# Performance work log

Measured on AMD Instinct MI355X. Metric: run time of the kernel, lower is better.

## Reference

```python
import jax, jax.numpy as jnp
import numpy as np

C64 = jnp.complex64


def _rot_mats(theta):
    """Return (RX, RY, RZ) 2x2 complex matrices for half-angle convention."""
    c = jnp.cos(theta / 2).astype(C64)
    s = jnp.sin(theta / 2).astype(C64)
    i = jnp.asarray(1j, C64)
    rx = jnp.stack([jnp.stack([c, -i * s]), jnp.stack([-i * s, c])])
    ry = jnp.stack([jnp.stack([c, -s]), jnp.stack([s, c])])
    e = jnp.exp(-i * theta.astype(C64) / 2)
    z0 = jnp.asarray(0.0, C64)
    rz = jnp.stack([jnp.stack([e, z0]), jnp.stack([z0, jnp.conj(e)])])
    return rx, ry, rz


def _apply_1q(state, U, wire):
    # state: [N,2,2,2,2]; apply U on qubit axis (1+wire)
    state = jnp.moveaxis(state, 1 + wire, 4)
    state = jnp.einsum('ab,nijkb->nijka', U, state)
    return jnp.moveaxis(state, 4, 1 + wire)


def _apply_cnot(state, ctrl, tgt):
    state = jnp.moveaxis(state, (1 + ctrl, 1 + tgt), (3, 4))
    s0 = state[..., 0, :]
    s1 = state[..., 1, ::-1]  # flip target where control=1
    state = jnp.stack([s0, s1], axis=3)
    return jnp.moveaxis(state, (3, 4), (1 + ctrl, 1 + tgt))


def _quanvolution(x, q_params):
    B = x.shape[0]
    img = x.reshape(B, 28, 28)
    # 2x2 non-overlapping patches, row-major: [B,196,4] with order (r,c),(r,c+1),(r+1,c),(r+1,c+1)
    patches = img.reshape(B, 14, 2, 14, 2).transpose(0, 1, 3, 2, 4).reshape(B * 196, 4)
    # RY encoding on |0>: per-wire vector [cos(t/2), sin(t/2)] -> product state
    half = patches / 2
    v = jnp.stack([jnp.cos(half), jnp.sin(half)], axis=-1).astype(C64)  # [N,4,2]
    state = jnp.einsum('na,nb,nc,nd->nabcd', v[:, 0], v[:, 1], v[:, 2], v[:, 3])
    # fixed 8-op random layer: 5 parameterized rotations + 3 CNOTs
    rx0, _, _ = _rot_mats(q_params[0])
    _, ry1, _ = _rot_mats(q_params[1])
    _, _, rz2 = _rot_mats(q_params[2])
    rx3, _, _ = _rot_mats(q_params[3])
    _, ry4, _ = _rot_mats(q_params[4])
    state = _apply_1q(state, rx0, 0)
    state = _apply_1q(state, ry1, 1)
    state = _apply_1q(state, rz2, 2)
    state = _apply_cnot(state, 0, 1)
    state = _apply_1q(state, rx3, 3)
    state = _apply_cnot(state, 2, 3)
    state = _apply_1q(state, ry4, 0)
    state = _apply_cnot(state, 1, 2)
    probs = state.real ** 2 + state.imag ** 2  # [N,2,2,2,2]
    z = jnp.array([1.0, -1.0], jnp.float32)
    exps = jnp.stack([
        jnp.einsum('nabcd,a->n', probs, z),
        jnp.einsum('nabcd,b->n', probs, z),
        jnp.einsum('nabcd,c->n', probs, z),
        jnp.einsum('nabcd,d->n', probs, z),
    ], axis=-1)  # [N,4], PauliZ per wire
    return exps.reshape(B, 196 * 4)


def setup_inputs() -> dict:
    key = jax.random.key(0)
    k0, k1, k2, k3 = jax.random.split(key, 4)
    B = 4096
    x = jax.random.uniform(k0, (B, 1, 28, 28), dtype=jnp.float32)
    q_params = jax.random.normal(k1, (5,), dtype=jnp.float32)
    W1 = jax.random.normal(k2, (128, 784), dtype=jnp.float32) * 0.02
    b1 = jnp.zeros((128,), jnp.float32)
    W2 = jax.random.normal(k3, (10, 128), dtype=jnp.float32) * 0.02
    b2 = jnp.zeros((10,), jnp.float32)
    return {"x": x, "q_params": q_params, "W1": W1, "b1": b1, "W2": W2, "b2": b2}


def reference(x, q_params, W1, b1, W2, b2):
    feats = _quanvolution(x, q_params)              # [B, 784]
    hidden = jax.nn.relu(feats @ W1.T + b1)          # [B, 128]
    logits = hidden @ W2.T + b2                      # [B, 10]
    return logits
```

## Files before the change

### kernel.cpp

```cpp
#include <hip/hip_runtime.h>

#define NB 4096
#define NPATCH 196
#define KP 800

typedef __attribute__((ext_vector_type(8))) short short8;
typedef __attribute__((ext_vector_type(4))) float f32x4;

__device__ __forceinline__ ushort f2bf(float f) {
    unsigned b = __builtin_bit_cast(unsigned, f);
    b += 0x7FFFu + ((b >> 16) & 1u);
    return (ushort)(b >> 16);
}

__global__ __launch_bounds__(256) void conv_kernel(
    const float* __restrict__ W1, const float* __restrict__ W2,
    const float* __restrict__ qp,
    ushort* __restrict__ W1b, ushort* __restrict__ W2b,
    float* __restrict__ gtab)
{
    int t = blockIdx.x * 256 + threadIdx.x;
    if (blockIdx.x == 0 && threadIdx.x < 10) {
        int q = threadIdx.x >> 1;
        float h = 0.5f * qp[q];
        gtab[threadIdx.x] = (threadIdx.x & 1) ? __cosf(h) : __sinf(h);
    }
    if (t < 128 * KP) {
        int r = t / KP, k = t - r * KP;
        W1b[t] = (k < 784) ? f2bf(W1[r * 784 + k]) : (ushort)0;
    } else {
        int u = t - 128 * KP;
        if (u < 16 * 128) W2b[u] = (u < 1280) ? f2bf(W2[u]) : (ushort)0;
    }
}

__global__ __launch_bounds__(256) void quanv_kernel(
    const float* __restrict__ x, const float* __restrict__ gtab,
    ushort* __restrict__ fb)
{
    int t = blockIdx.x * 256 + threadIdx.x;
    if (t >= NB * NPATCH) return;
    int b = t / NPATCH;
    int p = t - b * NPATCH;
    int pi = p / 14;
    int pj = p - pi * 14;

    const float* img = x + b * 784 + (2 * pi) * 28 + 2 * pj;
    float2 top = *reinterpret_cast<const float2*>(img);
    float2 bot = *reinterpret_cast<const float2*>(img + 28);
    float ang[4] = {top.x, top.y, bot.x, bot.y};

    float vc[4], vs[4];
#pragma unroll
    for (int q = 0; q < 4; ++q) {
        vs[q] = __sinf(0.5f * ang[q]);
        vc[q] = __cosf(0.5f * ang[q]);
    }

    float re[16], im[16];
#pragma unroll
    for (int i = 0; i < 16; ++i) {
        re[i] = ((i & 8) ? vs[0] : vc[0]) * ((i & 4) ? vs[1] : vc[1]) *
                ((i & 2) ? vs[2] : vc[2]) * ((i & 1) ? vs[3] : vc[3]);
        im[i] = 0.0f;
    }

    float gc, gs;

    gs = gtab[0]; gc = gtab[1];
#pragma unroll
    for (int i = 0; i < 16; ++i) if (!(i & 8)) {
        int j = i | 8;
        float r0 = re[i], i0 = im[i], r1 = re[j], i1 = im[j];
        re[i] = gc * r0 + gs * i1; im[i] = gc * i0 - gs * r1;
        re[j] = gc * r1 + gs * i0; im[j] = gc * i1 - gs * r0;
    }
    gs = gtab[2]; gc = gtab[3];
#pragma unroll
    for (int i = 0; i < 16; ++i) if (!(i & 4)) {
        int j = i | 4;
        float r0 = re[i], i0 = im[i], r1 = re[j], i1 = im[j];
        re[i] = gc * r0 - gs * r1; im[i] = gc * i0 - gs * i1;
        re[j] = gs * r0 + gc * r1; im[j] = gs * i0 + gc * i1;
    }
    gs = gtab[4]; gc = gtab[5];
#pragma unroll
    for (int i = 0; i < 16; ++i) if (!(i & 2)) {
        int j = i | 2;
        float r0 = re[i], i0 = im[i], r1 = re[j], i1 = im[j];
        re[i] = gc * r0 + gs * i0; im[i] = gc * i0 - gs * r0;
        re[j] = gc * r1 - gs * i1; im[j] = gc * i1 + gs * r1;
    }
#pragma unroll
    for (int i = 0; i < 16; ++i) if ((i & 8) && !(i & 4)) {
        int j = i | 4;
        float tr = re[i], ti = im[i];
        re[i] = re[j]; im[i] = im[j];
        re[j] = tr;    im[j] = ti;
    }
    gs = gtab[6]; gc = gtab[7];
#pragma unroll
    for (int i = 0; i < 16; ++i) if (!(i & 1)) {
        int j = i | 1;
        float r0 = re[i], i0 = im[i], r1 = re[j], i1 = im[j];
        re[i] = gc * r0 + gs * i1; im[i] = gc * i0 - gs * r1;
        re[j] = gc * r1 + gs * i0; im[j] = gc * i1 - gs * r0;
    }
#pragma unroll
    for (int i = 0; i < 16; ++i) if ((i & 2) && !(i & 1)) {
        int j = i | 1;
        float tr = re[i], ti = im[i];
        re[i] = re[j]; im[i] = im[j];
        re[j] = tr;    im[j] = ti;
    }
    gs = gtab[8]; gc = gtab[9];
#pragma unroll
    for (int i = 0; i < 16; ++i) if (!(i & 8)) {
        int j = i | 8;
        float r0 = re[i], i0 = im[i], r1 = re[j], i1 = im[j];
        re[i] = gc * r0 - gs * r1; im[i] = gc * i0 - gs * i1;
        re[j] = gs * r0 + gc * r1; im[j] = gs * i0 + gc * i1;
    }
#pragma unroll
    for (int i = 0; i < 16; ++i) if ((i & 4) && !(i & 2)) {
        int j = i | 2;
        float tr = re[i], ti = im[i];
        re[i] = re[j]; im[i] = im[j];
        re[j] = tr;    im[j] = ti;
    }

    float e0 = 0.f, e1 = 0.f, e2 = 0.f, e3 = 0.f;
#pragma unroll
    for (int i = 0; i < 16; ++i) {
        float pr = re[i] * re[i] + im[i] * im[i];
        e0 += (i & 8) ? -pr : pr;
        e1 += (i & 4) ? -pr : pr;
        e2 += (i & 2) ? -pr : pr;
        e3 += (i & 1) ? -pr : pr;
    }
    ushort4 o;
    o.x = f2bf(e0); o.y = f2bf(e1); o.z = f2bf(e2); o.w = f2bf(e3);
    *reinterpret_cast<ushort4*>(fb + b * KP + p * 4) = o;
    if (p < 4)
        *reinterpret_cast<ushort4*>(fb + b * KP + 784 + p * 4) = make_ushort4(0, 0, 0, 0);
}

__global__ __launch_bounds__(256) void mlp_mfma(
    const ushort* __restrict__ fb, const ushort* __restrict__ W1b,
    const float* __restrict__ b1, const ushort* __restrict__ W2b,
    const float* __restrict__ b2, float* __restrict__ out)
{
    __shared__ ushort Hs[16][136];

    const int t = threadIdx.x;
    const int l = t & 63;
    const int w = t >> 6;
    const int m0 = blockIdx.x * 16;
    const int row = l & 15;
    const int kg = l >> 4;

    f32x4 acc0 = {}, acc1 = {};
    const short8* ap  = reinterpret_cast<const short8*>(fb + (m0 + row) * KP + kg * 8);
    const short8* bp0 = reinterpret_cast<const short8*>(W1b + (w * 32 + row) * KP + kg * 8);
    const short8* bp1 = reinterpret_cast<const short8*>(W1b + (w * 32 + 16 + row) * KP + kg * 8);

    short8 A[2][5], B0[2][5], B1[2][5];
#pragma unroll
    for (int s = 0; s < 5; ++s) {
        A[0][s] = ap[s * 4]; B0[0][s] = bp0[s * 4]; B1[0][s] = bp1[s * 4];
    }
#pragma unroll
    for (int c = 0; c < 5; ++c) {
        const int cb = c & 1, nb = cb ^ 1;
        if (c < 4) {
#pragma unroll
            for (int s = 0; s < 5; ++s) {
                int ks = (c + 1) * 5 + s;
                A[nb][s]  = ap[ks * 4];
                B0[nb][s] = bp0[ks * 4];
                B1[nb][s] = bp1[ks * 4];
            }
        }
#pragma unroll
        for (int s = 0; s < 5; ++s) {
            acc0 = __builtin_amdgcn_mfma_f32_16x16x32_bf16(A[cb][s], B0[cb][s], acc0, 0, 0, 0);
            acc1 = __builtin_amdgcn_mfma_f32_16x16x32_bf16(A[cb][s], B1[cb][s], acc1, 0, 0, 0);
        }
    }

    {
        int cc0 = w * 32 + row, cc1 = cc0 + 16;
        float bj0 = b1[cc0], bj1 = b1[cc1];
#pragma unroll
        for (int r = 0; r < 4; ++r) {
            int rr = kg * 4 + r;
            Hs[rr][cc0] = f2bf(fmaxf(acc0[r] + bj0, 0.0f));
            Hs[rr][cc1] = f2bf(fmaxf(acc1[r] + bj1, 0.0f));
        }
    }
    __syncthreads();

    if (w == 0) {
        f32x4 acc2 = {};
#pragma unroll
        for (int ks = 0; ks < 4; ++ks) {
            short8 a = *reinterpret_cast<const short8*>(&Hs[row][ks * 32 + kg * 8]);
            short8 b = *reinterpret_cast<const short8*>(W2b + row * 128 + ks * 32 + kg * 8);
            acc2 = __builtin_amdgcn_mfma_f32_16x16x32_bf16(a, b, acc2, 0, 0, 0);
        }
        if (row < 10) {
            float bj = b2[row];
#pragma unroll
            for (int r = 0; r < 4; ++r)
                out[(m0 + kg * 4 + r) * 10 + row] = acc2[r] + bj;
        }
    }
}

extern "C" void kernel_launch(void* const* d_in, const int* in_sizes, int n_in,
                              void* d_out, int out_size, void* d_ws, size_t ws_size,
                              hipStream_t stream)
{
    const float* x  = (const float*)d_in[0];
    const float* qp = (const float*)d_in[1];
    const float* W1 = (const float*)d_in[2];
    const float* b1 = (const float*)d_in[3];
    const float* W2 = (const float*)d_in[4];
    const float* b2 = (const float*)d_in[5];
    float* out = (float*)d_out;

    ushort* fb  = (ushort*)d_ws;
    ushort* W1b = fb + NB * KP;
    ushort* W2b = W1b + 128 * KP;
    float*  gtab = (float*)(W2b + 16 * 128);

    conv_kernel<<<(128 * KP + 16 * 128 + 255) / 256, 256, 0, stream>>>(W1, W2, qp, W1b, W2b, gtab);
    quanv_kernel<<<(NB * NPATCH + 255) / 256, 256, 0, stream>>>(x, gtab, fb);
    mlp_mfma<<<NB / 16, 256, 0, stream>>>(fb, W1b, b1, W2b, b2, out);
}
```

Measured before the change: 88.42 us.

## Replace 16-amplitude statevector simulation with closed-form PauliZ expectations

```diff
diff --git a/kernel.cpp b/kernel.cpp
--- a/kernel.cpp
+++ b/kernel.cpp
@@ -20,10 +20,11 @@
     float* __restrict__ gtab)
 {
     int t = blockIdx.x * 256 + threadIdx.x;
-    if (blockIdx.x == 0 && threadIdx.x < 10) {
-        int q = threadIdx.x >> 1;
-        float h = 0.5f * qp[q];
-        gtab[threadIdx.x] = (threadIdx.x & 1) ? __cosf(h) : __sinf(h);
+    if (t == 0) {
+        gtab[0] = __sinf(0.5f * qp[0]); gtab[1] = __cosf(0.5f * qp[0]);
+        gtab[2] = __sinf(0.5f * qp[1]); gtab[3] = __cosf(0.5f * qp[1]);
+        gtab[4] = __sinf(0.5f * qp[4]); gtab[5] = __cosf(0.5f * qp[4]);
+        gtab[6] = __cosf(qp[3]);
     }
     if (t < 128 * KP) {
         int r = t / KP, k = t - r * KP;
@@ -48,98 +49,36 @@
     const float* img = x + b * 784 + (2 * pi) * 28 + 2 * pj;
     float2 top = *reinterpret_cast<const float2*>(img);
     float2 bot = *reinterpret_cast<const float2*>(img + 28);
-    float ang[4] = {top.x, top.y, bot.x, bot.y};
 
-    float vc[4], vs[4];
-#pragma unroll
-    for (int q = 0; q < 4; ++q) {
-        vs[q] = __sinf(0.5f * ang[q]);
-        vc[q] = __cosf(0.5f * ang[q]);
-    }
+    float gs0 = gtab[0], gc0 = gtab[1];
+    float gs1 = gtab[2], gc1 = gtab[3];
+    float gs4 = gtab[4], gc4 = gtab[5];
+    float ct3 = gtab[6];
 
-    float re[16], im[16];
-#pragma unroll
-    for (int i = 0; i < 16; ++i) {
-        re[i] = ((i & 8) ? vs[0] : vc[0]) * ((i & 4) ? vs[1] : vc[1]) *
-                ((i & 2) ? vs[2] : vc[2]) * ((i & 1) ? vs[3] : vc[3]);
-        im[i] = 0.0f;
-    }
+    float c0 = __cosf(0.5f * top.x), s0 = __sinf(0.5f * top.x);
+    float c1 = __cosf(0.5f * top.y), s1 = __sinf(0.5f * top.y);
+    float cz2 = __cosf(bot.x);
+    float cz3 = __cosf(bot.y);
 
-    float gc, gs;
+    float P = gc0 * c0, Q = gs0 * s0, m = gc0 * s0, n = gs0 * c0;
+    float v0 = gc1 * c1 - gs1 * s1;
+    float v1 = gs1 * c1 + gc1 * s1;
 
-    gs = gtab[0]; gc = gtab[1];
-#pragma unroll
-    for (int i = 0; i < 16; ++i) if (!(i & 8)) {
-        int j = i | 8;
-        float r0 = re[i], i0 = im[i], r1 = re[j], i1 = im[j];
-        re[i] = gc * r0 + gs * i1; im[i] = gc * i0 - gs * r1;
-        re[j] = gc * r1 + gs * i0; im[j] = gc * i1 - gs * r0;
-    }
-    gs = gtab[2]; gc = gtab[3];
-#pragma unroll
-    for (int i = 0; i < 16; ++i) if (!(i & 4)) {
-        int j = i | 4;
-        float r0 = re[i], i0 = im[i], r1 = re[j], i1 = im[j];
-        re[i] = gc * r0 - gs * r1; im[i] = gc * i0 - gs * i1;
-        re[j] = gs * r0 + gc * r1; im[j] = gs * i0 + gc * i1;
-    }
-    gs = gtab[4]; gc = gtab[5];
-#pragma unroll
-    for (int i = 0; i < 16; ++i) if (!(i & 2)) {
-        int j = i | 2;
-        float r0 = re[i], i0 = im[i], r1 = re[j], i1 = im[j];
-        re[i] = gc * r0 + gs * i0; im[i] = gc * i0 - gs * r0;
-        re[j] = gc * r1 - gs * i1; im[j] = gc * i1 + gs * r1;
-    }
-#pragma unroll
-    for (int i = 0; i < 16; ++i) if ((i & 8) && !(i & 4)) {
-        int j = i | 4;
-        float tr = re[i], ti = im[i];
-        re[i] = re[j]; im[i] = im[j];
-        re[j] = tr;    im[j] = ti;
-    }
-    gs = gtab[6]; gc = gtab[7];
-#pragma unroll
-    for (int i = 0; i < 16; ++i) if (!(i & 1)) {
-        int j = i | 1;
-        float r0 = re[i], i0 = im[i], r1 = re[j], i1 = im[j];
-        re[i] = gc * r0 + gs * i1; im[i] = gc * i0 - gs * r1;
-        re[j] = gc * r1 + gs * i0; im[j] = gc * i1 - gs * r0;
-    }
-#pragma unroll
-    for (int i = 0; i < 16; ++i) if ((i & 2) && !(i & 1)) {
-        int j = i | 1;
-        float tr = re[i], ti = im[i];
-        re[i] = re[j]; im[i] = im[j];
-        re[j] = tr;    im[j] = ti;
-    }
-    gs = gtab[8]; gc = gtab[9];
-#pragma unroll
-    for (int i = 0; i < 16; ++i) if (!(i & 8)) {
-        int j = i | 8;
-        float r0 = re[i], i0 = im[i], r1 = re[j], i1 = im[j];
-        re[i] = gc * r0 - gs * r1; im[i] = gc * i0 - gs * i1;
-        re[j] = gs * r0 + gc * r1; im[j] = gs * i0 + gc * i1;
-    }
-#pragma unroll
-    for (int i = 0; i < 16; ++i) if ((i & 4) && !(i & 2)) {
-        int j = i | 2;
-        float tr = re[i], ti = im[i];
-        re[i] = re[j]; im[i] = im[j];
-        re[j] = tr;    im[j] = ti;
-    }
+    float a0 = gc4 * v0, b0 = gs4 * v1, g0 = gs4 * v0, d0 = gc4 * v1;
+    float r, i2;
+    r = a0 * P - b0 * m; i2 = a0 * Q - b0 * n; float P00 = r * r + i2 * i2;
+    r = g0 * P + d0 * m; i2 = g0 * Q + d0 * n; float P10 = r * r + i2 * i2;
+    float a1 = gc4 * v1, b1 = gs4 * v0, g1 = gs4 * v1, d1 = gc4 * v0;
+    r = a1 * P - b1 * m; i2 = a1 * Q - b1 * n; float P01 = r * r + i2 * i2;
+    r = g1 * P + d1 * m; i2 = g1 * Q + d1 * n; float P11 = r * r + i2 * i2;
 
-    float e0 = 0.f, e1 = 0.f, e2 = 0.f, e3 = 0.f;
-#pragma unroll
-    for (int i = 0; i < 16; ++i) {
-        float pr = re[i] * re[i] + im[i] * im[i];
-        e0 += (i & 8) ? -pr : pr;
-        e1 += (i & 4) ? -pr : pr;
-        e2 += (i & 2) ? -pr : pr;
-        e3 += (i & 1) ? -pr : pr;
-    }
+    float z0 = (P00 + P01) - (P10 + P11);
+    float z1 = (P00 + P10) - (P01 + P11);
+    float z2 = z1 * cz2;
+    float z3 = ct3 * cz3 * cz2;
+
     ushort4 o;
-    o.x = f2bf(e0); o.y = f2bf(e1); o.z = f2bf(e2); o.w = f2bf(e3);
+    o.x = f2bf(z0); o.y = f2bf(z1); o.z = f2bf(z2); o.w = f2bf(z3);
     *reinterpret_cast<ushort4*>(fb + b * KP + p * 4) = o;
     if (p < 4)
         *reinterpret_cast<ushort4*>(fb + b * KP + 784 + p * 4) = make_ushort4(0, 0, 0, 0);
```

After: 80.16 us. 9.3% less time.
